# Optimization experiments

Measured on AMD Instinct MI355X. Metric: run time of the kernel, lower is better.

Reference implementation:

```python
import jax, jax.numpy as jnp
import numpy as np

DIM = 2048
HEADS = 16
DIM_HEAD = 128
DIM_INNER = HEADS * DIM_HEAD
BATCH = 2
SEQ = 2048
EPS = 1e-12  # F.normalize default eps


def l2norm(t, axis=-1):
    # matches F.normalize(t, dim=axis, p=2): t / max(||t||, eps)
    n = jnp.sqrt(jnp.sum(t * t, axis=axis, keepdims=True))
    return t / jnp.maximum(n, EPS)


def setup_inputs() -> dict:
    key = jax.random.key(0)
    ks = jax.random.split(key, 5)
    x = jax.random.normal(ks[0], (BATCH, SEQ, DIM), dtype=jnp.float32)
    # NormLinear weights (torch Linear layout: [out, in]); parametrization
    # l2-normalizes rows (dim=-1) for q/k/v and columns (dim=0) for to_out.
    Wq = jax.random.normal(ks[1], (DIM_INNER, DIM), dtype=jnp.float32) / np.sqrt(DIM)
    Wk = jax.random.normal(ks[2], (DIM_INNER, DIM), dtype=jnp.float32) / np.sqrt(DIM)
    Wv = jax.random.normal(ks[3], (DIM_INNER, DIM), dtype=jnp.float32) / np.sqrt(DIM)
    Wout = jax.random.normal(ks[4], (DIM, DIM_INNER), dtype=jnp.float32) / np.sqrt(DIM_INNER)
    # Scale(dim_inner, init=1.0, scale=dim**-1): param = ones * dim**-1,
    # forward_scale = init/scale = dim, so qk_scale() starts at 1.0
    qk_scale = jnp.ones((DIM_INNER,), dtype=jnp.float32) / DIM
    return {"x": x, "Wq": Wq, "Wk": Wk, "Wv": Wv, "Wout": Wout, "qk_scale": qk_scale}


def reference(x, Wq, Wk, Wv, Wout, qk_scale):
    b, n, _ = x.shape
    # NormLinear: x @ l2norm(W, rows).T  (scale = groups**-1 = 1)
    q = jnp.einsum('bnd,ed->bne', x, l2norm(Wq, axis=-1))
    k = jnp.einsum('bnd,ed->bne', x, l2norm(Wk, axis=-1))
    v = jnp.einsum('bnd,ed->bne', x, l2norm(Wv, axis=-1))
    # split heads: b n (h d) -> b h n d
    split = lambda t: t.reshape(b, n, HEADS, DIM_HEAD).transpose(0, 2, 1, 3)
    q, k, v = split(q), split(k), split(v)
    # per-head l2norm of q and k over head dim
    q = l2norm(q, axis=-1)
    k = l2norm(k, axis=-1)
    # learned qk scale: (h d) -> h 1 d, effective = param * forward_scale(=DIM)
    q = q * (qk_scale * DIM).reshape(HEADS, 1, DIM_HEAD)
    # causal SDPA with scale = sqrt(dim_head) (unit-norm q,k in nGPT)
    attn_scale = DIM_HEAD ** 0.5
    scores = jnp.einsum('bhid,bhjd->bhij', q, k) * attn_scale
    causal = jnp.tril(jnp.ones((n, n), dtype=bool))
    scores = jnp.where(causal, scores, jnp.finfo(scores.dtype).min)
    attn = jax.nn.softmax(scores, axis=-1)
    out = jnp.einsum('bhij,bhjd->bhid', attn, v)
    # merge heads: b h n d -> b n (h d)
    out = out.transpose(0, 2, 1, 3).reshape(b, n, DIM_INNER)
    # to_out: NormLinear with norm over dim=0 of weight [DIM, DIM_INNER]
    out = jnp.einsum('bne,de->bnd', out, l2norm(Wout, axis=0))
    return out
```

## Files before the change

kernel.cpp:

```cpp
#include <hip/hip_runtime.h>


typedef __bf16 bf16x8 __attribute__((ext_vector_type(8)));
typedef float f32x4 __attribute__((ext_vector_type(4)));

__device__ __forceinline__ unsigned short f2bf(float f) {
  unsigned int u = __float_as_uint(f);
  u = u + 0x7FFFu + ((u >> 16) & 1u);
  return (unsigned short)(u >> 16);
}

__device__ __forceinline__ void async16(const void* g, void* l) {
  __builtin_amdgcn_global_load_lds(
      (const __attribute__((address_space(1))) unsigned int*)g,
      (__attribute__((address_space(3))) unsigned int*)l, 16, 0, 0);
}

#define QFOLD (2048.0f * 11.313708498984761f * 1.4426950408889634f)


__global__ __launch_bounds__(256) void prep_w_rows(
    const float* __restrict__ Wq, const float* __restrict__ Wk,
    const float* __restrict__ Wv, ushort* __restrict__ oq,
    ushort* __restrict__ ok_, ushort* __restrict__ ov) {
  const int row = blockIdx.x;
  const float* W = (blockIdx.y == 0) ? Wq : (blockIdx.y == 1) ? Wk : Wv;
  ushort* O = (blockIdx.y == 0) ? oq : (blockIdx.y == 1) ? ok_ : ov;
  const int t = threadIdx.x;
  const float4* Wr = (const float4*)(W + (size_t)row * 2048);
  float4 v0 = Wr[t];
  float4 v1 = Wr[t + 256];
  float ss = v0.x * v0.x + v0.y * v0.y + v0.z * v0.z + v0.w * v0.w +
             v1.x * v1.x + v1.y * v1.y + v1.z * v1.z + v1.w * v1.w;
  ss += __shfl_xor(ss, 1);  ss += __shfl_xor(ss, 2);
  ss += __shfl_xor(ss, 4);  ss += __shfl_xor(ss, 8);
  ss += __shfl_xor(ss, 16); ss += __shfl_xor(ss, 32);
  __shared__ float red[4];
  if ((t & 63) == 0) red[t >> 6] = ss;
  __syncthreads();
  float tot = red[0] + red[1] + red[2] + red[3];
  float sc = 1.0f / fmaxf(sqrtf(tot), 1e-12f);
  ushort4 o0, o1;
  o0.x = f2bf(v0.x * sc); o0.y = f2bf(v0.y * sc);
  o0.z = f2bf(v0.z * sc); o0.w = f2bf(v0.w * sc);
  o1.x = f2bf(v1.x * sc); o1.y = f2bf(v1.y * sc);
  o1.z = f2bf(v1.z * sc); o1.w = f2bf(v1.w * sc);
  *(ushort4*)(O + (size_t)row * 2048 + t * 4) = o0;
  *(ushort4*)(O + (size_t)row * 2048 + 1024 + t * 4) = o1;
}

__global__ __launch_bounds__(256) void wout_colss(const float* __restrict__ W,
                                                  float* __restrict__ colss) {
  const int e = blockIdx.x * 256 + threadIdx.x;
  const int d0 = blockIdx.y * 128;
  float ss = 0.f;
  #pragma unroll 8
  for (int i = 0; i < 128; ++i) {
    float v = W[(size_t)(d0 + i) * 2048 + e];
    ss += v * v;
  }
  atomicAdd(colss + e, ss);
}

__global__ __launch_bounds__(256) void wout_norm(const float* __restrict__ W,
                                                 const float* __restrict__ colss,
                                                 ushort* __restrict__ O) {
  const int idx = (blockIdx.x * 256 + threadIdx.x) * 4;
  float4 v = *(const float4*)(W + idx);
  float4 c = *(const float4*)(colss + (idx & 2047));
  ushort4 o;
  o.x = f2bf(v.x / fmaxf(sqrtf(c.x), 1e-12f));
  o.y = f2bf(v.y / fmaxf(sqrtf(c.y), 1e-12f));
  o.z = f2bf(v.z / fmaxf(sqrtf(c.z), 1e-12f));
  o.w = f2bf(v.w / fmaxf(sqrtf(c.w), 1e-12f));
  *(ushort4*)(O + idx) = o;
}

__global__ __launch_bounds__(256) void convert_x(const float* __restrict__ X,
                                                 ushort* __restrict__ O) {
  const int idx = (blockIdx.x * 256 + threadIdx.x) * 4;
  float4 v = *(const float4*)(X + idx);
  ushort4 o;
  o.x = f2bf(v.x); o.y = f2bf(v.y); o.z = f2bf(v.z); o.w = f2bf(v.w);
  *(ushort4*)(O + idx) = o;
}

__global__ __launch_bounds__(64) void qk_mhead(const float* __restrict__ qks,
                                               float* __restrict__ mh) {
  const int h = blockIdx.x, l = threadIdx.x;
  float m = fmaxf(fabsf(qks[h * 128 + l]), fabsf(qks[h * 128 + 64 + l]));
  m = fmaxf(m, __shfl_xor(m, 1));  m = fmaxf(m, __shfl_xor(m, 2));
  m = fmaxf(m, __shfl_xor(m, 4));  m = fmaxf(m, __shfl_xor(m, 8));
  m = fmaxf(m, __shfl_xor(m, 16)); m = fmaxf(m, __shfl_xor(m, 32));
  if (l == 0) mh[h] = m * QFOLD;
}

__device__ __forceinline__ void gemm_mainloop(
    const ushort* __restrict__ A, const ushort* __restrict__ Bw,
    int m0, int n0, ushort* As, ushort* Bs, f32x4 acc[4][4],
    int t, int l, int wm, int wn) {
  const int l15 = l & 15, l4 = l >> 4;
  const ushort* abase = A + (size_t)m0 * 2048;
  const ushort* bbase = Bw + (size_t)n0 * 2048;
  for (int kt = 0; kt < 32; ++kt) {
    const int k0 = kt * 64;
    __syncthreads();
    #pragma unroll
    for (int p = 0; p < 9; ++p) {
      int c = p * 256 + t;
      const ushort* src = abase;
      char* dst = (char*)As;
      int cc = c;
      if (c >= 1152) { cc = c - 1152; src = bbase; dst = (char*)Bs; }
      int r = cc / 9, dc = cc - r * 9;
      int dcc = (dc == 8) ? 0 : dc;
      async16(src + (size_t)r * 2048 + k0 + dcc * 8, dst + cc * 16);
    }
    __syncthreads();
    #pragma unroll
    for (int ks = 0; ks < 2; ++ks) {
      bf16x8 af[4], bg[4];
      #pragma unroll
      for (int f = 0; f < 4; ++f)
        af[f] = *(const bf16x8*)&As[(wm * 64 + f * 16 + l15) * 72 + ks * 32 + l4 * 8];
      #pragma unroll
      for (int f = 0; f < 4; ++f)
        bg[f] = *(const bf16x8*)&Bs[(wn * 64 + f * 16 + l15) * 72 + ks * 32 + l4 * 8];
      #pragma unroll
      for (int fm = 0; fm < 4; ++fm)
        #pragma unroll
        for (int fn = 0; fn < 4; ++fn)
          acc[fm][fn] = __builtin_amdgcn_mfma_f32_16x16x32_bf16(
              af[fm], bg[fn], acc[fm][fn], 0, 0, 0);
    }
  }
}

__global__ __launch_bounds__(256, 4) void gemm_qkv(
    const ushort* __restrict__ X, const ushort* __restrict__ Wq,
    const ushort* __restrict__ Wk, const ushort* __restrict__ Wv,
    const float* __restrict__ qks, ushort* __restrict__ qn,
    ushort* __restrict__ kn, ushort* __restrict__ vt) {
  const int z = blockIdx.z;
  const ushort* Bw = (z == 0) ? Wq : (z == 1) ? Wk : Wv;
  const int n0 = blockIdx.x * 128;
  const int m0 = blockIdx.y * 128;
  __shared__ __align__(16) ushort As[128 * 72];
  __shared__ __align__(16) ushort Bs[128 * 72];
  __shared__ float partials[2][128];
  const int t = threadIdx.x, w = t >> 6, l = t & 63;
  const int wm = w & 1, wn = w >> 1;
  const int l15 = l & 15, l4 = l >> 4;

  f32x4 acc[4][4];
  #pragma unroll
  for (int i = 0; i < 4; ++i)
    #pragma unroll
    for (int j = 0; j < 4; ++j) acc[i][j] = (f32x4){0.f, 0.f, 0.f, 0.f};

  gemm_mainloop(X, Bw, m0, n0, As, Bs, acc, t, l, wm, wn);

  const int h = n0 >> 7;
  if (z == 2) {
    #pragma unroll
    for (int fm = 0; fm < 4; ++fm) {
      int mrow = m0 + wm * 64 + fm * 16 + l4 * 4;
      int bb = mrow >> 11;
      int nn = mrow & 2047;
      #pragma unroll
      for (int fn = 0; fn < 4; ++fn) {
        int d = wn * 64 + fn * 16 + l15;
        ushort4 p;
        p.x = f2bf(acc[fm][fn][0]); p.y = f2bf(acc[fm][fn][1]);
        p.z = f2bf(acc[fm][fn][2]); p.w = f2bf(acc[fm][fn][3]);
        *(ushort4*)(vt + (size_t)((bb * 16 + h) * 128 + d) * 2048 + nn) = p;
      }
    }
  } else {
    float rs[4][4];
    #pragma unroll
    for (int fm = 0; fm < 4; ++fm)
      #pragma unroll
      for (int r = 0; r < 4; ++r) {
        float s = 0.f;
        #pragma unroll
        for (int fn = 0; fn < 4; ++fn) {
          float v = acc[fm][fn][r];
          s += v * v;
        }
        s += __shfl_xor(s, 1); s += __shfl_xor(s, 2);
        s += __shfl_xor(s, 4); s += __shfl_xor(s, 8);
        rs[fm][r] = s;
      }
    if (l15 == 0) {
      #pragma unroll
      for (int fm = 0; fm < 4; ++fm)
        #pragma unroll
        for (int r = 0; r < 4; ++r)
          partials[wn][wm * 64 + fm * 16 + l4 * 4 + r] = rs[fm][r];
    }
    __syncthreads();
    float cs[4];
    #pragma unroll
    for (int fn = 0; fn < 4; ++fn)
      cs[fn] = (z == 0) ? qks[n0 + wn * 64 + fn * 16 + l15] * QFOLD : 1.0f;
    ushort* O = (z == 0) ? qn : kn;
    #pragma unroll
    for (int fm = 0; fm < 4; ++fm)
      #pragma unroll
      for (int r = 0; r < 4; ++r) {
        int i = wm * 64 + fm * 16 + l4 * 4 + r;
        float tot = partials[0][i] + partials[1][i];
        float sc = 1.0f / fmaxf(sqrtf(tot), 1e-12f);
        #pragma unroll
        for (int fn = 0; fn < 4; ++fn)
          O[(size_t)(m0 + i) * 2048 + n0 + wn * 64 + fn * 16 + l15] =
              f2bf(acc[fm][fn][r] * sc * cs[fn]);
      }
  }
}

__device__ __forceinline__ void attn_stage(const ushort* kbase,
                                           const ushort* vbase, int j0,
                                           ushort* Kb, ushort* Vb, int t) {
  #pragma unroll
  for (int p = 0; p < 4; ++p) {
    int c = p * 256 + t;
    int j = c >> 4, ch = c & 15;
    int g = (ch & 8) | ((ch ^ j) & 7);
    async16(kbase + (size_t)(j0 + j) * 2048 + g * 8, (char*)Kb + c * 16);
  }
  #pragma unroll
  for (int p = 0; p < 4; ++p) {
    int c = p * 256 + t;
    int d = c >> 3, ch = c & 7;
    int g = (ch ^ d) & 7;
    async16(vbase + (size_t)d * 2048 + j0 + g * 8, (char*)Vb + c * 16);
  }
}

__global__ __launch_bounds__(256, 2) void attn_kernel(
    const ushort* __restrict__ qn, const ushort* __restrict__ kn,
    const ushort* __restrict__ vt, const float* __restrict__ mhead,
    ushort* __restrict__ ao) {
  const int hb = blockIdx.x;
  const int b = hb >> 4, h = hb & 15;
  const int y = blockIdx.y;
  const int qt = (y < 8) ? (15 - y) : (y - 8);
  const int i0 = qt * 128;
  const int t = threadIdx.x, w = t >> 6, l = t & 63;
  const int l15 = l & 15, l4 = l >> 4;

  __shared__ __align__(16) ushort Ks[2][64 * 128];
  __shared__ __align__(16) ushort Vts[2][128 * 64];
  __shared__ __align__(16) ushort Ps[128 * 64];

  bf16x8 qf[2][4];
  #pragma unroll
  for (int fi = 0; fi < 2; ++fi)
    #pragma unroll
    for (int ks = 0; ks < 4; ++ks)
      qf[fi][ks] = *(const bf16x8*)(qn +
          (size_t)(b * 2048 + i0 + w * 32 + fi * 16 + l15) * 2048 +
          h * 128 + ks * 32 + l4 * 8);

  f32x4 Oa[2][8];
  #pragma unroll
  for (int fi = 0; fi < 2; ++fi)
    #pragma unroll
    for (int fd = 0; fd < 8; ++fd) Oa[fi][fd] = (f32x4){0.f, 0.f, 0.f, 0.f};
  f32x4 Ol[2];
  Ol[0] = (f32x4){0.f, 0.f, 0.f, 0.f};
  Ol[1] = (f32x4){0.f, 0.f, 0.f, 0.f};

  const float mh = mhead[h];
  const __bf16 one = (__bf16)1.0f;
  const bf16x8 ones = {one, one, one, one, one, one, one, one};

  const ushort* kbase = kn + (size_t)(b * 2048) * 2048 + h * 128;
  const ushort* vbase = vt + (size_t)((b * 16 + h) * 128) * 2048;
  const int jt_end = 2 * qt + 2;

  attn_stage(kbase, vbase, 0, Ks[0], Vts[0], t);

  for (int jt = 0; jt < jt_end; ++jt) {
    const int buf = jt & 1;
    const int j0 = jt * 64;
    __syncthreads();
    if (jt + 1 < jt_end)
      attn_stage(kbase, vbase, (jt + 1) * 64, Ks[buf ^ 1], Vts[buf ^ 1], t);

    f32x4 Sa[2][4];
    #pragma unroll
    for (int fj = 0; fj < 4; ++fj) {
      f32x4 s0 = (f32x4){0.f, 0.f, 0.f, 0.f};
      f32x4 s1 = (f32x4){0.f, 0.f, 0.f, 0.f};
      #pragma unroll
      for (int ks = 0; ks < 4; ++ks) {
        int g = ks * 4 + l4;
        int phys = (g & 8) | ((g ^ l15) & 7);
        bf16x8 kf = *(const bf16x8*)&Ks[buf][(fj * 16 + l15) * 128 + phys * 8];
        s0 = __builtin_amdgcn_mfma_f32_16x16x32_bf16(qf[0][ks], kf, s0, 0, 0, 0);
        s1 = __builtin_amdgcn_mfma_f32_16x16x32_bf16(qf[1][ks], kf, s1, 0, 0, 0);
      }
      Sa[0][fj] = s0; Sa[1][fj] = s1;
    }

    if (jt >= 2 * qt) {
      #pragma unroll
      for (int fi = 0; fi < 2; ++fi)
        #pragma unroll
        for (int fj = 0; fj < 4; ++fj)
          #pragma unroll
          for (int r = 0; r < 4; ++r) {
            int jg = j0 + fj * 16 + l15;
            int ig = i0 + w * 32 + fi * 16 + l4 * 4 + r;
            if (jg > ig) Sa[fi][fj][r] = -1e30f;
          }
    }

    #pragma unroll
    for (int fi = 0; fi < 2; ++fi)
      #pragma unroll
      for (int fj = 0; fj < 4; ++fj) {
        int cj = fj * 2 + (l15 >> 3);
        #pragma unroll
        for (int r = 0; r < 4; ++r) {
          int i = w * 32 + fi * 16 + l4 * 4 + r;
          Ps[i * 64 + ((cj ^ i) & 7) * 8 + (l15 & 7)] =
              f2bf(__builtin_exp2f(Sa[fi][fj][r] - mh));
        }
      }

    #pragma unroll
    for (int ks = 0; ks < 2; ++ks) {
      int sw = ((ks * 4 + l4) ^ l15) & 7;
      bf16x8 p0 = *(const bf16x8*)&Ps[(w * 32 + l15) * 64 + sw * 8];
      bf16x8 p1 = *(const bf16x8*)&Ps[(w * 32 + 16 + l15) * 64 + sw * 8];
      Ol[0] = __builtin_amdgcn_mfma_f32_16x16x32_bf16(p0, ones, Ol[0], 0, 0, 0);
      Ol[1] = __builtin_amdgcn_mfma_f32_16x16x32_bf16(p1, ones, Ol[1], 0, 0, 0);
      #pragma unroll
      for (int fd = 0; fd < 8; ++fd) {
        bf16x8 vf = *(const bf16x8*)&Vts[buf][(fd * 16 + l15) * 64 + sw * 8];
        Oa[0][fd] = __builtin_amdgcn_mfma_f32_16x16x32_bf16(p0, vf, Oa[0][fd], 0, 0, 0);
        Oa[1][fd] = __builtin_amdgcn_mfma_f32_16x16x32_bf16(p1, vf, Oa[1][fd], 0, 0, 0);
      }
    }
  }

  #pragma unroll
  for (int fi = 0; fi < 2; ++fi)
    #pragma unroll
    for (int r = 0; r < 4; ++r) {
      float inv = 1.0f / Ol[fi][r];
      int ig = i0 + w * 32 + fi * 16 + l4 * 4 + r;
      #pragma unroll
      for (int fd = 0; fd < 8; ++fd)
        ao[(size_t)(b * 2048 + ig) * 2048 + h * 128 + fd * 16 + l15] =
            f2bf(Oa[fi][fd][r] * inv);
    }
}

__global__ __launch_bounds__(256, 4) void gemm_out(
    const ushort* __restrict__ A, const ushort* __restrict__ Bw,
    float* __restrict__ C) {
  const int n0 = blockIdx.x * 128;
  const int m0 = blockIdx.y * 128;
  __shared__ __align__(16) ushort As[128 * 72];
  __shared__ __align__(16) ushort Bs[128 * 72];
  const int t = threadIdx.x, w = t >> 6, l = t & 63;
  const int wm = w & 1, wn = w >> 1;
  const int l15 = l & 15, l4 = l >> 4;

  f32x4 acc[4][4];
  #pragma unroll
  for (int i = 0; i < 4; ++i)
    #pragma unroll
    for (int j = 0; j < 4; ++j) acc[i][j] = (f32x4){0.f, 0.f, 0.f, 0.f};

  gemm_mainloop(A, Bw, m0, n0, As, Bs, acc, t, l, wm, wn);

  #pragma unroll
  for (int fm = 0; fm < 4; ++fm)
    #pragma unroll
    for (int fn = 0; fn < 4; ++fn)
      #pragma unroll
      for (int r = 0; r < 4; ++r)
        C[(size_t)(m0 + wm * 64 + fm * 16 + l4 * 4 + r) * 2048 +
          n0 + wn * 64 + fn * 16 + l15] = acc[fm][fn][r];
}

extern "C" void kernel_launch(void* const* d_in, const int* in_sizes, int n_in,
                              void* d_out, int out_size, void* d_ws, size_t ws_size,
                              hipStream_t stream) {
  (void)in_sizes; (void)n_in; (void)out_size; (void)ws_size;
  const float* x    = (const float*)d_in[0];
  const float* Wq   = (const float*)d_in[1];
  const float* Wk   = (const float*)d_in[2];
  const float* Wv   = (const float*)d_in[3];
  const float* Wout = (const float*)d_in[4];
  const float* qks  = (const float*)d_in[5];
  char* ws = (char*)d_ws;

  ushort* wqn  = (ushort*)(ws + 0);
  ushort* wkn  = (ushort*)(ws + 8388608);
  ushort* wvn  = (ushort*)(ws + 16777216);
  ushort* wotn = (ushort*)(ws + 25165824);
  ushort* xbf  = (ushort*)(ws + 33554432);
  ushort* qn   = (ushort*)(ws + 50331648);
  ushort* kn   = (ushort*)(ws + 67108864);
  ushort* vt   = (ushort*)(ws + 83886080);
  ushort* ao   = (ushort*)(ws + 100663296);
  float* colss = (float*)(ws + 117440512);
  float* mh    = (float*)(ws + 117448704);
  float* out   = (float*)d_out;

  hipMemsetAsync(colss, 0, 2048 * sizeof(float), stream);
  prep_w_rows<<<dim3(2048, 3), 256, 0, stream>>>(Wq, Wk, Wv, wqn, wkn, wvn);
  wout_colss<<<dim3(8, 16), 256, 0, stream>>>(Wout, colss);
  wout_norm<<<4096, 256, 0, stream>>>(Wout, colss, wotn);
  convert_x<<<8192, 256, 0, stream>>>(x, xbf);
  qk_mhead<<<16, 64, 0, stream>>>(qks, mh);
  gemm_qkv<<<dim3(16, 32, 3), 256, 0, stream>>>(xbf, wqn, wkn, wvn, qks, qn, kn, vt);
  attn_kernel<<<dim3(32, 16), 256, 0, stream>>>(qn, kn, vt, mh, ao);
  gemm_out<<<dim3(16, 32), 256, 0, stream>>>(ao, wotn, out);
}
```

Baseline: 395.0 us.

## Keep attention probabilities in registers via transposed QK^T and drop the LDS P buffer

```diff
diff --git a/kernel.cpp b/kernel.cpp
--- a/kernel.cpp
+++ b/kernel.cpp
@@ -2,6 +2,7 @@
 
 
 typedef __bf16 bf16x8 __attribute__((ext_vector_type(8)));
+typedef __bf16 bf16x4 __attribute__((ext_vector_type(4)));
 typedef float f32x4 __attribute__((ext_vector_type(4)));
 
 __device__ __forceinline__ unsigned short f2bf(float f) {
@@ -220,25 +221,6 @@
   }
 }
 
-__device__ __forceinline__ void attn_stage(const ushort* kbase,
-                                           const ushort* vbase, int j0,
-                                           ushort* Kb, ushort* Vb, int t) {
-  #pragma unroll
-  for (int p = 0; p < 4; ++p) {
-    int c = p * 256 + t;
-    int j = c >> 4, ch = c & 15;
-    int g = (ch & 8) | ((ch ^ j) & 7);
-    async16(kbase + (size_t)(j0 + j) * 2048 + g * 8, (char*)Kb + c * 16);
-  }
-  #pragma unroll
-  for (int p = 0; p < 4; ++p) {
-    int c = p * 256 + t;
-    int d = c >> 3, ch = c & 7;
-    int g = (ch ^ d) & 7;
-    async16(vbase + (size_t)d * 2048 + j0 + g * 8, (char*)Vb + c * 16);
-  }
-}
-
 __global__ __launch_bounds__(256, 2) void attn_kernel(
     const ushort* __restrict__ qn, const ushort* __restrict__ kn,
     const ushort* __restrict__ vt, const float* __restrict__ mhead,
@@ -251,9 +233,8 @@
   const int t = threadIdx.x, w = t >> 6, l = t & 63;
   const int l15 = l & 15, l4 = l >> 4;
 
-  __shared__ __align__(16) ushort Ks[2][64 * 128];
-  __shared__ __align__(16) ushort Vts[2][128 * 64];
-  __shared__ __align__(16) ushort Ps[128 * 64];
+  __shared__ __align__(16) ushort Ks[64 * 128];
+  __shared__ __align__(16) ushort Vts[128 * 72];
 
   bf16x8 qf[2][4];
   #pragma unroll
@@ -281,69 +262,70 @@
   const ushort* vbase = vt + (size_t)((b * 16 + h) * 128) * 2048;
   const int jt_end = 2 * qt + 2;
 
-  attn_stage(kbase, vbase, 0, Ks[0], Vts[0], t);
-
   for (int jt = 0; jt < jt_end; ++jt) {
-    const int buf = jt & 1;
     const int j0 = jt * 64;
     __syncthreads();
-    if (jt + 1 < jt_end)
-      attn_stage(kbase, vbase, (jt + 1) * 64, Ks[buf ^ 1], Vts[buf ^ 1], t);
-
-    f32x4 Sa[2][4];
-    #pragma unroll
-    for (int fj = 0; fj < 4; ++fj) {
-      f32x4 s0 = (f32x4){0.f, 0.f, 0.f, 0.f};
-      f32x4 s1 = (f32x4){0.f, 0.f, 0.f, 0.f};
-      #pragma unroll
-      for (int ks = 0; ks < 4; ++ks) {
-        int g = ks * 4 + l4;
-        int phys = (g & 8) | ((g ^ l15) & 7);
-        bf16x8 kf = *(const bf16x8*)&Ks[buf][(fj * 16 + l15) * 128 + phys * 8];
-        s0 = __builtin_amdgcn_mfma_f32_16x16x32_bf16(qf[0][ks], kf, s0, 0, 0, 0);
-        s1 = __builtin_amdgcn_mfma_f32_16x16x32_bf16(qf[1][ks], kf, s1, 0, 0, 0);
-      }
-      Sa[0][fj] = s0; Sa[1][fj] = s1;
-    }
-
-    if (jt >= 2 * qt) {
-      #pragma unroll
-      for (int fi = 0; fi < 2; ++fi)
-        #pragma unroll
-        for (int fj = 0; fj < 4; ++fj)
+    #pragma unroll
+    for (int p = 0; p < 4; ++p) {
+      int c = p * 256 + t;
+      int j = c >> 4, ch = c & 15;
+      int g = (ch & 8) | ((ch ^ j) & 7);
+      async16(kbase + (size_t)(j0 + j) * 2048 + g * 8, (char*)Ks + c * 16);
+    }
+    #pragma unroll
+    for (int p = 0; p < 5; ++p) {
+      int c = p * 256 + t;
+      if (c < 1152) {
+        int r = c / 9, jc = c - r * 9;
+        int jcc = (jc == 8) ? 0 : jc;
+        async16(vbase + (size_t)r * 2048 + j0 + jcc * 8, (char*)Vts + c * 16);
+      }
+    }
+    __syncthreads();
+
+    #pragma unroll
+    for (int fjp = 0; fjp < 2; ++fjp) {
+      bf16x8 P[2];
+      #pragma unroll
+      for (int fje = 0; fje < 2; ++fje) {
+        const int fj = fjp * 2 + fje;
+        f32x4 St[2];
+        St[0] = (f32x4){0.f, 0.f, 0.f, 0.f};
+        St[1] = (f32x4){0.f, 0.f, 0.f, 0.f};
+        #pragma unroll
+        for (int ks = 0; ks < 4; ++ks) {
+          int g = ks * 4 + l4;
+          int phys = (g & 8) | ((g ^ l15) & 7);
+          bf16x8 kf = *(const bf16x8*)&Ks[(fj * 16 + l15) * 128 + phys * 8];
+          St[0] = __builtin_amdgcn_mfma_f32_16x16x32_bf16(kf, qf[0][ks], St[0], 0, 0, 0);
+          St[1] = __builtin_amdgcn_mfma_f32_16x16x32_bf16(kf, qf[1][ks], St[1], 0, 0, 0);
+        }
+        if (jt >= 2 * qt) {
           #pragma unroll
-          for (int r = 0; r < 4; ++r) {
-            int jg = j0 + fj * 16 + l15;
-            int ig = i0 + w * 32 + fi * 16 + l4 * 4 + r;
-            if (jg > ig) Sa[fi][fj][r] = -1e30f;
-          }
-    }
-
-    #pragma unroll
-    for (int fi = 0; fi < 2; ++fi)
-      #pragma unroll
-      for (int fj = 0; fj < 4; ++fj) {
-        int cj = fj * 2 + (l15 >> 3);
-        #pragma unroll
-        for (int r = 0; r < 4; ++r) {
-          int i = w * 32 + fi * 16 + l4 * 4 + r;
-          Ps[i * 64 + ((cj ^ i) & 7) * 8 + (l15 & 7)] =
-              f2bf(__builtin_exp2f(Sa[fi][fj][r] - mh));
+          for (int fi = 0; fi < 2; ++fi)
+            #pragma unroll
+            for (int r = 0; r < 4; ++r) {
+              int jg = j0 + fj * 16 + l4 * 4 + r;
+              int ig = i0 + w * 32 + fi * 16 + l15;
+              if (jg > ig) St[fi][r] = -1e30f;
+            }
         }
-      }
-
-    #pragma unroll
-    for (int ks = 0; ks < 2; ++ks) {
-      int sw = ((ks * 4 + l4) ^ l15) & 7;
-      bf16x8 p0 = *(const bf16x8*)&Ps[(w * 32 + l15) * 64 + sw * 8];
-      bf16x8 p1 = *(const bf16x8*)&Ps[(w * 32 + 16 + l15) * 64 + sw * 8];
-      Ol[0] = __builtin_amdgcn_mfma_f32_16x16x32_bf16(p0, ones, Ol[0], 0, 0, 0);
-      Ol[1] = __builtin_amdgcn_mfma_f32_16x16x32_bf16(p1, ones, Ol[1], 0, 0, 0);
+        #pragma unroll
+        for (int fi = 0; fi < 2; ++fi)
+          #pragma unroll
+          for (int r = 0; r < 4; ++r)
+            P[fi][fje * 4 + r] = (__bf16)__builtin_exp2f(St[fi][r] - mh);
+      }
+      Ol[0] = __builtin_amdgcn_mfma_f32_16x16x32_bf16(P[0], ones, Ol[0], 0, 0, 0);
+      Ol[1] = __builtin_amdgcn_mfma_f32_16x16x32_bf16(P[1], ones, Ol[1], 0, 0, 0);
       #pragma unroll
       for (int fd = 0; fd < 8; ++fd) {
-        bf16x8 vf = *(const bf16x8*)&Vts[buf][(fd * 16 + l15) * 64 + sw * 8];
-        Oa[0][fd] = __builtin_amdgcn_mfma_f32_16x16x32_bf16(p0, vf, Oa[0][fd], 0, 0, 0);
-        Oa[1][fd] = __builtin_amdgcn_mfma_f32_16x16x32_bf16(p1, vf, Oa[1][fd], 0, 0, 0);
+        const int row = fd * 16 + l15;
+        bf16x4 v0 = *(const bf16x4*)&Vts[row * 72 + fjp * 32 + l4 * 4];
+        bf16x4 v1 = *(const bf16x4*)&Vts[row * 72 + fjp * 32 + 16 + l4 * 4];
+        bf16x8 vf = __builtin_shufflevector(v0, v1, 0, 1, 2, 3, 4, 5, 6, 7);
+        Oa[0][fd] = __builtin_amdgcn_mfma_f32_16x16x32_bf16(P[0], vf, Oa[0][fd], 0, 0, 0);
+        Oa[1][fd] = __builtin_amdgcn_mfma_f32_16x16x32_bf16(P[1], vf, Oa[1][fd], 0, 0, 0);
       }
     }
   }
```

Result: no change. 401.3 us (+1.6%).
